# Optimization experiments

Measured on AMD Instinct MI355X. Metric: run time of the kernel, lower is better.

## Reference

```python
import jax, jax.numpy as jnp
import numpy as np

N = 65536       # tokens (voxels)
C = 128         # dim
H = 4           # num_heads
HD = C // H     # head_dim = 32
NUM_WIN = 1024  # number of windows


def setup_inputs() -> dict:
    key = jax.random.key(0)
    k1, k2, k3, k4 = jax.random.split(key, 4)
    x = jax.random.normal(k1, (N, C), dtype=jnp.float32)
    w_qkv = jax.random.normal(k2, (3 * C, C), dtype=jnp.float32) * 0.02
    w_proj = jax.random.normal(k3, (C, C), dtype=jnp.float32) * 0.02
    b_proj = jnp.zeros((C,), dtype=jnp.float32)
    batch_win_inds = jnp.sort(jax.random.randint(k4, (N,), 0, NUM_WIN)).astype(jnp.int32)
    counts = jax.ops.segment_sum(jnp.ones((N,), jnp.int32), batch_win_inds, num_segments=NUM_WIN)
    offsets = jnp.concatenate([jnp.zeros((1,), jnp.int32), jnp.cumsum(counts)]).astype(jnp.int32)
    return {"x": x, "w_qkv": w_qkv, "w_proj": w_proj, "b_proj": b_proj,
            "batch_win_inds": batch_win_inds, "offsets": offsets, "counts": counts}


def reference(x, w_qkv, w_proj, b_proj, batch_win_inds, offsets, counts):
    # qkv projection (no bias), split, per-head reshape
    qkv = (x @ w_qkv.T).reshape(N, 3, H, HD)          # [N,3,H,HD]
    q = jax.nn.relu(qkv[:, 0])                        # [N,H,HD]
    k = jax.nn.relu(qkv[:, 1])                        # [N,H,HD]
    v = qkv[:, 2]                                     # [N,H,HD]

    kv = jax.ops.segment_sum(
        jnp.einsum('nhc,nhd->nhcd', k, v), batch_win_inds, num_segments=NUM_WIN)
    # per-window key sum s[w,h,c]
    s = jax.ops.segment_sum(k, batch_win_inds, num_segments=NUM_WIN)

    y = jnp.einsum('nhc,nhcd->nhd', q, kv[batch_win_inds])
    z = jnp.sum(s[batch_win_inds] * q, axis=-1, keepdims=True)
    y = y / (z + 1e-6)

    y = y.reshape(N, C)
    return y @ w_proj.T + b_proj
```

## Files before the change

kernel.cpp:

```cpp
#include <hip/hip_runtime.h>

namespace {
constexpr int C     = 128;
constexpr int T     = 64;
constexpr int BLK   = 512;
constexpr int NWIN  = 1024;
constexpr int KVSTR = 40;
constexpr int KTSTR = 72;
constexpr int YNSTR = 136;
constexpr int WSPN  = 131072;
constexpr size_t QN = (size_t)65536 * 128;
}

typedef __attribute__((ext_vector_type(8))) short bf16x8;
typedef __attribute__((ext_vector_type(4))) short sh4;
typedef __attribute__((ext_vector_type(4))) float f32x4;

__device__ __forceinline__ short bf16rne(float f) {
    unsigned u = __float_as_uint(f);
    u += 0x7fffu + ((u >> 16) & 1u);
    return (short)(u >> 16);
}
__device__ __forceinline__ float bf16f(short h) {
    return __uint_as_float(((unsigned)(unsigned short)h) << 16);
}
__device__ __forceinline__ void split1(float f, short& hi, short& lo) {
    hi = bf16rne(f);
    lo = bf16rne(f - bf16f(hi));
}

__global__ void prep_weights(const float* __restrict__ wqkv,
                             const float* __restrict__ wproj,
                             short* __restrict__ wsp) {
    const int i = blockIdx.x * 256 + threadIdx.x;
    const float f = (i < 49152) ? wqkv[i] : wproj[i - 49152];
    short hi, lo;
    split1(f, hi, lo);
    wsp[i] = hi;
    wsp[65536 + i] = lo;
}

__global__ __launch_bounds__(BLK, 2)
void qkv_gemm(const float* __restrict__ x,
              const short* __restrict__ wsp,
              short* __restrict__ qws,
              short* __restrict__ kws,
              short* __restrict__ vws)
{
    __shared__ __align__(16) short xh[64 * YNSTR];
    __shared__ __align__(16) short xl[64 * YNSTR];

    const int tid = threadIdx.x;
    const int wv = tid >> 6, ln = tid & 63;
    const int fr = ln & 15, fg = ln >> 4;
    const int r0 = blockIdx.x * 64;

#pragma unroll
    for (int it = 0; it < 2; ++it) {
        const int i = tid + it * BLK;
        const int t = i >> 4, c8 = (i & 15) << 3;
        const float* p = x + (size_t)(r0 + t) * C + c8;
        const float4 a = *(const float4*)p;
        const float4 b = *(const float4*)(p + 4);
        const float f[8] = {a.x, a.y, a.z, a.w, b.x, b.y, b.z, b.w};
        bf16x8 hi, lo;
#pragma unroll
        for (int u = 0; u < 8; ++u) { short h_, l_; split1(f[u], h_, l_); hi[u] = h_; lo[u] = l_; }
        *(bf16x8*)(xh + t * YNSTR + c8) = hi;
        *(bf16x8*)(xl + t * YNSTR + c8) = lo;
    }
    __syncthreads();

    f32x4 acc[3][4];
#pragma unroll
    for (int ni = 0; ni < 3; ++ni)
#pragma unroll
        for (int m = 0; m < 4; ++m) acc[ni][m] = f32x4{0.f, 0.f, 0.f, 0.f};

#pragma unroll
    for (int ksi = 0; ksi < 4; ++ksi) {
        const int koff = ksi * 32 + fg * 8;
        bf16x8 ahi[4], alo[4];
#pragma unroll
        for (int m = 0; m < 4; ++m) {
            const int row = m * 16 + fr;
            ahi[m] = *(const bf16x8*)(xh + row * YNSTR + koff);
            alo[m] = *(const bf16x8*)(xl + row * YNSTR + koff);
        }
#pragma unroll
        for (int ni = 0; ni < 3; ++ni) {
            const int idx = ((3 * wv + ni) * 16 + fr) * C + koff;
            const bf16x8 bhi = *(const bf16x8*)(wsp + idx);
            const bf16x8 blo = *(const bf16x8*)(wsp + 65536 + idx);
#pragma unroll
            for (int m = 0; m < 4; ++m) {
                acc[ni][m] = __builtin_amdgcn_mfma_f32_16x16x32_bf16(ahi[m], bhi, acc[ni][m], 0, 0, 0);
                acc[ni][m] = __builtin_amdgcn_mfma_f32_16x16x32_bf16(ahi[m], blo, acc[ni][m], 0, 0, 0);
                acc[ni][m] = __builtin_amdgcn_mfma_f32_16x16x32_bf16(alo[m], bhi, acc[ni][m], 0, 0, 0);
            }
        }
    }

    const int trow = tid >> 3;
    const int toff = (tid & 7) << 4;
#pragma unroll
    for (int p = 0; p < 3; ++p) {
        __syncthreads();
#pragma unroll
        for (int ni = 0; ni < 3; ++ni) {
            const int ti = 3 * wv + ni;
            if ((ti >> 3) == p) {
                const int lc = (ti - 8 * p) * 16 + fr;
                const bool rl = (p < 2);
#pragma unroll
                for (int m = 0; m < 4; ++m)
#pragma unroll
                    for (int e = 0; e < 4; ++e) {
                        float v = acc[ni][m][e];
                        if (rl) v = fmaxf(v, 0.f);
                        xh[(m * 16 + fg * 4 + e) * YNSTR + lc] = bf16rne(v);
                    }
            }
        }
        __syncthreads();
        short* dst = (p == 0) ? qws : ((p == 1) ? kws : vws);
        const bf16x8 o0 = *(const bf16x8*)(xh + trow * YNSTR + toff);
        const bf16x8 o1 = *(const bf16x8*)(xh + trow * YNSTR + toff + 8);
        *(bf16x8*)(dst + (size_t)(r0 + trow) * C + toff) = o0;
        *(bf16x8*)(dst + (size_t)(r0 + trow) * C + toff + 8) = o1;
    }
}

__global__ __launch_bounds__(BLK, 2)
void sla_win(const short* __restrict__ qws,
             const short* __restrict__ kws,
             const short* __restrict__ vws,
             const short* __restrict__ wsp,
             const float* __restrict__ bproj,
             const int*   __restrict__ offsets,
             float*       __restrict__ out)
{
    __shared__ __align__(16) short kT[C * KTSTR];
    __shared__ __align__(16) short vT[C * KTSTR];
    __shared__ __align__(16) short yn[T * YNSTR];
    __shared__ __align__(16) short kvs[4 * 32 * KVSTR];
    __shared__ float ss[C];

    const int win = blockIdx.x;
    const int beg = offsets[win];
    const int cnt = offsets[win + 1] - beg;
    if (cnt <= 0) return;
    const int nch = (cnt + T - 1) / T;

    const int tid = threadIdx.x;
    const int wv = tid >> 6, ln = tid & 63;
    const int fr = ln & 15, fg = ln >> 4;
    const int aH = wv >> 1, tw = wv & 1;

    f32x4 kvacc[2] = {{0.f,0.f,0.f,0.f},{0.f,0.f,0.f,0.f}};
    f32x4 sacc = {0.f, 0.f, 0.f, 0.f};
    bf16x8 ones;
#pragma unroll
    for (int u = 0; u < 8; ++u) ones[u] = (short)0x3F80;

    for (int c0 = 0; c0 < nch; ++c0) {
        const int t0 = c0 * T;
        const int tc = (cnt - t0 < T) ? (cnt - t0) : T;

#pragma unroll
        for (int it = 0; it < 2; ++it) {
            const int i = tid + it * BLK;
            const int t = i >> 4, c8 = (i & 15) << 3;
            bf16x8 k8, v8;
#pragma unroll
            for (int u = 0; u < 8; ++u) { k8[u] = 0; v8[u] = 0; }
            if (t < tc) {
                k8 = *(const bf16x8*)(kws + (size_t)(beg + t0 + t) * C + c8);
                v8 = *(const bf16x8*)(vws + (size_t)(beg + t0 + t) * C + c8);
            }
#pragma unroll
            for (int u = 0; u < 8; ++u) {
                const int c = c8 + u;
                const int tt = t ^ (((c >> 3) & 7) << 3);
                kT[c * KTSTR + tt] = k8[u];
                vT[c * KTSTR + tt] = v8[u];
            }
        }
        __syncthreads();

        {
#pragma unroll
            for (int kt = 0; kt < 2; ++kt) {
                const int t8 = kt * 32 + fg * 8;
                const int cch = aH * 32 + tw * 16 + fr;
                const bf16x8 a8 = *(const bf16x8*)(kT + cch * KTSTR + (t8 ^ (((cch >> 3) & 7) << 3)));
                sacc = __builtin_amdgcn_mfma_f32_16x16x32_bf16(a8, ones, sacc, 0, 0, 0);
#pragma unroll
                for (int dt = 0; dt < 2; ++dt) {
                    const int dch = aH * 32 + dt * 16 + fr;
                    const bf16x8 b8 = *(const bf16x8*)(vT + dch * KTSTR + (t8 ^ (((dch >> 3) & 7) << 3)));
                    kvacc[dt] = __builtin_amdgcn_mfma_f32_16x16x32_bf16(a8, b8, kvacc[dt], 0, 0, 0);
                }
            }
        }
        if (c0 + 1 < nch) __syncthreads();
    }

    {
#pragma unroll
        for (int dt = 0; dt < 2; ++dt) {
            const int d = dt * 16 + fr;
#pragma unroll
            for (int e = 0; e < 4; ++e) {
                const int c = tw * 16 + fg * 4 + e;
                kvs[aH * (32 * KVSTR) + d * KVSTR + c] = bf16rne(kvacc[dt][e]);
            }
        }
        if (fr == 0) {
#pragma unroll
            for (int e = 0; e < 4; ++e)
                ss[aH * 32 + tw * 16 + fg * 4 + e] = sacc[e];
        }
    }
    __syncthreads();

    for (int c0 = 0; c0 < nch; ++c0) {
        const int t0 = c0 * T;
        const int tc = (cnt - t0 < T) ? (cnt - t0) : T;

        {
            const int a = wv >> 1, mp = wv & 1;
            bf16x8 bfr[2];
#pragma unroll
            for (int dl = 0; dl < 2; ++dl)
                bfr[dl] = *(const bf16x8*)(kvs + a * (32 * KVSTR) + (dl * 16 + fr) * KVSTR + fg * 8);

            const float4 s0 = *(const float4*)(ss + a * 32 + fg * 8);
            const float4 s1 = *(const float4*)(ss + a * 32 + fg * 8 + 4);

            bf16x8 afr[2];
            float zinv[2];
#pragma unroll
            for (int mi = 0; mi < 2; ++mi) {
                const int row = (mp * 2 + mi) * 16 + fr;
                afr[mi] = *(const bf16x8*)(qws + (size_t)(beg + t0 + row) * C + a * 32 + fg * 8);
                float zp = 0.f;
                zp = fmaf(bf16f(afr[mi][0]), s0.x, zp);
                zp = fmaf(bf16f(afr[mi][1]), s0.y, zp);
                zp = fmaf(bf16f(afr[mi][2]), s0.z, zp);
                zp = fmaf(bf16f(afr[mi][3]), s0.w, zp);
                zp = fmaf(bf16f(afr[mi][4]), s1.x, zp);
                zp = fmaf(bf16f(afr[mi][5]), s1.y, zp);
                zp = fmaf(bf16f(afr[mi][6]), s1.z, zp);
                zp = fmaf(bf16f(afr[mi][7]), s1.w, zp);
                zp += __shfl_xor(zp, 16);
                zp += __shfl_xor(zp, 32);
                zinv[mi] = 1.f / (zp + 1e-6f);
            }
            f32x4 acc[2][2];
#pragma unroll
            for (int mi = 0; mi < 2; ++mi)
#pragma unroll
                for (int dl = 0; dl < 2; ++dl) {
                    acc[mi][dl] = f32x4{0.f, 0.f, 0.f, 0.f};
                    acc[mi][dl] = __builtin_amdgcn_mfma_f32_16x16x32_bf16(afr[mi], bfr[dl], acc[mi][dl], 0, 0, 0);
                }
#pragma unroll
            for (int mi = 0; mi < 2; ++mi)
#pragma unroll
                for (int e = 0; e < 4; ++e) {
                    const float zt = __shfl(zinv[mi], fg * 4 + e);
                    const int t = (mp * 2 + mi) * 16 + fg * 4 + e;
#pragma unroll
                    for (int dl = 0; dl < 2; ++dl) {
                        const int ch = a * 32 + dl * 16 + fr;
                        yn[t * YNSTR + ch] = bf16rne(acc[mi][dl][e] * zt);
                    }
                }
        }
        __syncthreads();

        {
            f32x4 acc[4];
#pragma unroll
            for (int m = 0; m < 4; ++m) acc[m] = f32x4{0.f, 0.f, 0.f, 0.f};
#pragma unroll
            for (int ksi = 0; ksi < 4; ++ksi) {
                const int koff = ksi * 32 + fg * 8;
                bf16x8 a8[4];
#pragma unroll
                for (int m = 0; m < 4; ++m) {
                    const int row = m * 16 + fr;
                    a8[m] = *(const bf16x8*)(yn + row * YNSTR + koff);
                }
                const int idx = (384 + wv * 16 + fr) * C + koff;
                const bf16x8 bhi = *(const bf16x8*)(wsp + idx);
                const bf16x8 blo = *(const bf16x8*)(wsp + 65536 + idx);
#pragma unroll
                for (int m = 0; m < 4; ++m) {
                    acc[m] = __builtin_amdgcn_mfma_f32_16x16x32_bf16(a8[m], bhi, acc[m], 0, 0, 0);
                    acc[m] = __builtin_amdgcn_mfma_f32_16x16x32_bf16(a8[m], blo, acc[m], 0, 0, 0);
                }
            }
            const int ch = wv * 16 + fr;
            const float b = bproj[ch];
#pragma unroll
            for (int m = 0; m < 4; ++m)
#pragma unroll
                for (int e = 0; e < 4; ++e) {
                    const int t = m * 16 + fg * 4 + e;
                    if (t < tc)
                        out[(size_t)(beg + t0 + t) * C + ch] = acc[m][e] + b;
                }
        }
        if (c0 + 1 < nch) __syncthreads();
    }
}

__global__ __launch_bounds__(BLK, 2)
void sla6(const float* __restrict__ x, const float* __restrict__ bproj,
          const int* __restrict__ offsets, const short* __restrict__ wsp,
          short* __restrict__ qws, float* __restrict__ out)
{
    __shared__ __align__(16) short xs_hi[T * C];
    __shared__ __align__(16) short xs_lo[T * C];
    __shared__ __align__(16) short kT[C * T];
    __shared__ __align__(16) short vTy[C * T];
    __shared__ __align__(16) short kvs[4 * 32 * KVSTR];
    __shared__ float ss[C];

    const int win = blockIdx.x;
    const int beg = offsets[win];
    const int cnt = offsets[win + 1] - beg;
    if (cnt <= 0) return;
    const int nch = (cnt + T - 1) / T;

    const int tid = threadIdx.x;
    const int wv = tid >> 6, ln = tid & 63;
    const int fr = ln & 15, fg = ln >> 4;

    auto loadB = [&](int row512, int koff, bf16x8& bhi, bf16x8& blo) {
        const int idx = row512 * C + koff;
        bhi = *(const bf16x8*)(wsp + idx);
        blo = *(const bf16x8*)(wsp + 65536 + idx);
    };
    auto stage = [&](int t0, int tc) {
#pragma unroll
        for (int it = 0; it < 2; ++it) {
            const int i = tid + it * BLK;
            const int t = i >> 4, c8 = (i & 15) << 3;
            float4 a = {0.f, 0.f, 0.f, 0.f}, b = {0.f, 0.f, 0.f, 0.f};
            if (t < tc) {
                const float* p = x + (size_t)(beg + t0 + t) * C + c8;
                a = *(const float4*)p;
                b = *(const float4*)(p + 4);
            }
            const float f[8] = {a.x, a.y, a.z, a.w, b.x, b.y, b.z, b.w};
            bf16x8 hi, lo;
#pragma unroll
            for (int u = 0; u < 8; ++u) { short h_, l_; split1(f[u], h_, l_); hi[u] = h_; lo[u] = l_; }
            const int s = t * C + (c8 ^ ((t & 7) << 3));
            *(bf16x8*)(xs_hi + s) = hi;
            *(bf16x8*)(xs_lo + s) = lo;
        }
    };

    const int aH = wv >> 1, tw = wv & 1;
    f32x4 kvacc[2] = {{0.f,0.f,0.f,0.f},{0.f,0.f,0.f,0.f}};
    f32x4 sacc = {0.f, 0.f, 0.f, 0.f};
    bf16x8 ones;
#pragma unroll
    for (int u = 0; u < 8; ++u) ones[u] = (short)0x3F80;

    for (int c0 = 0; c0 < nch; ++c0) {
        const int t0 = c0 * T;
        const int tc = (cnt - t0 < T) ? (cnt - t0) : T;
        stage(t0, tc);
        __syncthreads();
        sh4 qreg[4];
        {
            f32x4 acc[2][4];
#pragma unroll
            for (int ni = 0; ni < 2; ++ni)
#pragma unroll
                for (int m = 0; m < 4; ++m) acc[ni][m] = f32x4{0.f, 0.f, 0.f, 0.f};
#pragma unroll
            for (int ksi = 0; ksi < 4; ++ksi) {
                const int koff = ksi * 32 + fg * 8;
                bf16x8 ahi[4], alo[4];
#pragma unroll
                for (int m = 0; m < 4; ++m) {
                    const int row = m * 16 + fr;
                    const int s = row * C + (koff ^ ((row & 7) << 3));
                    ahi[m] = *(const bf16x8*)(xs_hi + s);
                    alo[m] = *(const bf16x8*)(xs_lo + s);
                }
#pragma unroll
                for (int ni = 0; ni < 2; ++ni) {
                    bf16x8 bhi, blo;
                    loadB(128 + (2 * wv + ni) * 16 + fr, koff, bhi, blo);
#pragma unroll
                    for (int m = 0; m < 4; ++m) {
                        acc[ni][m] = __builtin_amdgcn_mfma_f32_16x16x32_bf16(ahi[m], bhi, acc[ni][m], 0, 0, 0);
                        acc[ni][m] = __builtin_amdgcn_mfma_f32_16x16x32_bf16(ahi[m], blo, acc[ni][m], 0, 0, 0);
                        acc[ni][m] = __builtin_amdgcn_mfma_f32_16x16x32_bf16(alo[m], bhi, acc[ni][m], 0, 0, 0);
                    }
                }
            }
#pragma unroll
            for (int ni = 0; ni < 2; ++ni) {
                const int nt = 2 * wv + ni;
                const bool isk = (nt < 8);
                const int ch = (isk ? nt : nt - 8) * 16 + fr;
                short* dst = isk ? kT : vTy;
#pragma unroll
                for (int m = 0; m < 4; ++m) {
                    sh4 h4;
#pragma unroll
                    for (int e = 0; e < 4; ++e) {
                        float v = acc[ni][m][e];
                        if (isk) v = fmaxf(v, 0.f);
                        h4[e] = bf16rne(v);
                    }
                    const int tb = m * 16 + fg * 4;
                    *(sh4*)(dst + ch * T + (tb ^ ((ch & 7) << 3))) = h4;
                }
            }
        }
        {
            f32x4 acc[4];
#pragma unroll
            for (int m = 0; m < 4; ++m) acc[m] = f32x4{0.f, 0.f, 0.f, 0.f};
#pragma unroll
            for (int ksi = 0; ksi < 4; ++ksi) {
                const int koff = ksi * 32 + fg * 8;
                bf16x8 ahi[4], alo[4];
#pragma unroll
                for (int m = 0; m < 4; ++m) {
                    const int row = m * 16 + fr;
                    const int s = row * C + (koff ^ ((row & 7) << 3));
                    ahi[m] = *(const bf16x8*)(xs_hi + s);
                    alo[m] = *(const bf16x8*)(xs_lo + s);
                }
                bf16x8 bhi, blo;
                loadB(wv * 16 + fr, koff, bhi, blo);
#pragma unroll
                for (int m = 0; m < 4; ++m) {
                    acc[m] = __builtin_amdgcn_mfma_f32_16x16x32_bf16(ahi[m], bhi, acc[m], 0, 0, 0);
                    acc[m] = __builtin_amdgcn_mfma_f32_16x16x32_bf16(ahi[m], blo, acc[m], 0, 0, 0);
                    acc[m] = __builtin_amdgcn_mfma_f32_16x16x32_bf16(alo[m], bhi, acc[m], 0, 0, 0);
                }
            }
#pragma unroll
            for (int m = 0; m < 4; ++m)
#pragma unroll
                for (int e = 0; e < 4; ++e)
                    qreg[m][e] = bf16rne(fmaxf(acc[m][e], 0.f));
        }
        __syncthreads();
        {
            const int ch = wv * 16 + fr;
            if (nch == 1) {
#pragma unroll
                for (int m = 0; m < 4; ++m)
#pragma unroll
                    for (int e = 0; e < 4; ++e) {
                        const int t = m * 16 + fg * 4 + e;
                        xs_hi[t * C + (ch ^ ((t & 7) << 3))] = qreg[m][e];
                    }
            } else {
#pragma unroll
                for (int m = 0; m < 4; ++m)
#pragma unroll
                    for (int e = 0; e < 4; ++e) {
                        const int t = m * 16 + fg * 4 + e;
                        if (t < tc)
                            qws[(size_t)(beg + t0 + t) * C + ch] = qreg[m][e];
                    }
            }
        }
        {
#pragma unroll
            for (int kt = 0; kt < 2; ++kt) {
                const int t8 = kt * 32 + fg * 8;
                const int cch = aH * 32 + tw * 16 + fr;
                const bf16x8 a8 = *(const bf16x8*)(kT + cch * T + (t8 ^ ((cch & 7) << 3)));
                sacc = __builtin_amdgcn_mfma_f32_16x16x32_bf16(a8, ones, sacc, 0, 0, 0);
#pragma unroll
                for (int dt = 0; dt < 2; ++dt) {
                    const int dch = aH * 32 + dt * 16 + fr;
                    const bf16x8 b8 = *(const bf16x8*)(vTy + dch * T + (t8 ^ ((dch & 7) << 3)));
                    kvacc[dt] = __builtin_amdgcn_mfma_f32_16x16x32_bf16(a8, b8, kvacc[dt], 0, 0, 0);
                }
            }
        }
        if (c0 + 1 < nch) __syncthreads();
    }
    {
#pragma unroll
        for (int dt = 0; dt < 2; ++dt) {
            const int d = dt * 16 + fr;
#pragma unroll
            for (int e = 0; e < 4; ++e) {
                const int c = tw * 16 + fg * 4 + e;
                kvs[aH * (32 * KVSTR) + d * KVSTR + c] = bf16rne(kvacc[dt][e]);
            }
        }
        if (fr == 0) {
#pragma unroll
            for (int e = 0; e < 4; ++e)
                ss[aH * 32 + tw * 16 + fg * 4 + e] = sacc[e];
        }
    }
    __syncthreads();
    for (int c0 = 0; c0 < nch; ++c0) {
        const int t0 = c0 * T;
        const int tc = (cnt - t0 < T) ? (cnt - t0) : T;
        {
            const int a = wv >> 1, mp = wv & 1;
            bf16x8 bfr[2];
#pragma unroll
            for (int dl = 0; dl < 2; ++dl)
                bfr[dl] = *(const bf16x8*)(kvs + a * (32 * KVSTR) + (dl * 16 + fr) * KVSTR + fg * 8);
            const float4 s0 = *(const float4*)(ss + a * 32 + fg * 8);
            const float4 s1 = *(const float4*)(ss + a * 32 + fg * 8 + 4);
            bf16x8 afr[2];
            float zinv[2];
#pragma unroll
            for (int mi = 0; mi < 2; ++mi) {
                const int row = (mp * 2 + mi) * 16 + fr;
                if (nch == 1)
                    afr[mi] = *(const bf16x8*)(xs_hi + row * C + ((a * 32 + fg * 8) ^ ((row & 7) << 3)));
                else
                    afr[mi] = *(const bf16x8*)(qws + (size_t)(beg + t0 + row) * C + a * 32 + fg * 8);
                float zp = 0.f;
                zp = fmaf(bf16f(afr[mi][0]), s0.x, zp);
                zp = fmaf(bf16f(afr[mi][1]), s0.y, zp);
                zp = fmaf(bf16f(afr[mi][2]), s0.z, zp);
                zp = fmaf(bf16f(afr[mi][3]), s0.w, zp);
                zp = fmaf(bf16f(afr[mi][4]), s1.x, zp);
                zp = fmaf(bf16f(afr[mi][5]), s1.y, zp);
                zp = fmaf(bf16f(afr[mi][6]), s1.z, zp);
                zp = fmaf(bf16f(afr[mi][7]), s1.w, zp);
                zp += __shfl_xor(zp, 16);
                zp += __shfl_xor(zp, 32);
                zinv[mi] = 1.f / (zp + 1e-6f);
            }
            f32x4 acc[2][2];
#pragma unroll
            for (int mi = 0; mi < 2; ++mi)
#pragma unroll
                for (int dl = 0; dl < 2; ++dl) {
                    acc[mi][dl] = f32x4{0.f, 0.f, 0.f, 0.f};
                    acc[mi][dl] = __builtin_amdgcn_mfma_f32_16x16x32_bf16(afr[mi], bfr[dl], acc[mi][dl], 0, 0, 0);
                }
#pragma unroll
            for (int mi = 0; mi < 2; ++mi)
#pragma unroll
                for (int e = 0; e < 4; ++e) {
                    const float zt = __shfl(zinv[mi], fg * 4 + e);
                    const int t = (mp * 2 + mi) * 16 + fg * 4 + e;
#pragma unroll
                    for (int dl = 0; dl < 2; ++dl) {
                        const int ch = a * 32 + dl * 16 + fr;
                        vTy[t * C + (ch ^ ((t & 7) << 3))] = bf16rne(acc[mi][dl][e] * zt);
                    }
                }
        }
        __syncthreads();
        {
            f32x4 acc[4];
#pragma unroll
            for (int m = 0; m < 4; ++m) acc[m] = f32x4{0.f, 0.f, 0.f, 0.f};
#pragma unroll
            for (int ksi = 0; ksi < 4; ++ksi) {
                const int koff = ksi * 32 + fg * 8;
                bf16x8 a8[4];
#pragma unroll
                for (int m = 0; m < 4; ++m) {
                    const int row = m * 16 + fr;
                    a8[m] = *(const bf16x8*)(vTy + row * C + (koff ^ ((row & 7) << 3)));
                }
                bf16x8 bhi, blo;
                loadB(384 + wv * 16 + fr, koff, bhi, blo);
#pragma unroll
                for (int m = 0; m < 4; ++m) {
                    acc[m] = __builtin_amdgcn_mfma_f32_16x16x32_bf16(a8[m], bhi, acc[m], 0, 0, 0);
                    acc[m] = __builtin_amdgcn_mfma_f32_16x16x32_bf16(a8[m], blo, acc[m], 0, 0, 0);
                }
            }
            const int ch = wv * 16 + fr;
            const float b = bproj[ch];
#pragma unroll
            for (int m = 0; m < 4; ++m)
#pragma unroll
                for (int e = 0; e < 4; ++e) {
                    const int t = m * 16 + fg * 4 + e;
                    if (t < tc)
                        out[(size_t)(beg + t0 + t) * C + ch] = acc[m][e] + b;
                }
        }
        if (c0 + 1 < nch) __syncthreads();
    }
}

extern "C" void kernel_launch(void* const* d_in, const int* in_sizes, int n_in,
                              void* d_out, int out_size, void* d_ws, size_t ws_size,
                              hipStream_t stream)
{
    const float* x       = (const float*)d_in[0];
    const float* wqkv    = (const float*)d_in[1];
    const float* wproj   = (const float*)d_in[2];
    const float* bproj   = (const float*)d_in[3];
    const int*   offsets = (const int*)d_in[5];
    float* out = (float*)d_out;
    short* wsp = (short*)d_ws;

    const size_t need_split = ((size_t)WSPN + 3 * QN) * sizeof(short);
    const size_t need_sla6  = ((size_t)WSPN + QN) * sizeof(short);

    if (ws_size >= need_split) {
        short* qws = wsp + WSPN;
        short* kws = qws + QN;
        short* vws = kws + QN;
        hipLaunchKernelGGL(prep_weights, dim3(256), dim3(256), 0, stream, wqkv, wproj, wsp);
        hipLaunchKernelGGL(qkv_gemm, dim3(65536 / 64), dim3(BLK), 0, stream,
                           x, wsp, qws, kws, vws);
        hipLaunchKernelGGL(sla_win, dim3(NWIN), dim3(BLK), 0, stream,
                           qws, kws, vws, wsp, bproj, offsets, out);
    } else if (ws_size >= need_sla6) {
        hipLaunchKernelGGL(prep_weights, dim3(256), dim3(256), 0, stream, wqkv, wproj, wsp);
        hipLaunchKernelGGL(sla6, dim3(NWIN), dim3(BLK), 0, stream,
                           x, bproj, offsets, wsp, wsp + WSPN, out);
    }
}
```

Before: 77.98 us.

## Keep QKV weight fragments in registers and process four row chunks per block

The QKV GEMM kernel now loads each wave's bf16 hi/lo weight fragments into registers once and reuses them across four 64-row chunks, so each block covers 256 rows and the grid shrinks to a quarter. The epilogue writes Q and K together using both shared buffers, then V, which cuts the number of barrier-separated phases. This removes repeated global weight loads per 64 rows. In exchange it uses many more registers (96 bf16x8 vectors), which could lower occupancy or cause spills, and it launches fewer blocks.

```diff
diff --git a/kernel.cpp b/kernel.cpp
--- a/kernel.cpp
+++ b/kernel.cpp
@@ -53,81 +53,115 @@
     const int tid = threadIdx.x;
     const int wv = tid >> 6, ln = tid & 63;
     const int fr = ln & 15, fg = ln >> 4;
-    const int r0 = blockIdx.x * 64;
-
-#pragma unroll
-    for (int it = 0; it < 2; ++it) {
-        const int i = tid + it * BLK;
-        const int t = i >> 4, c8 = (i & 15) << 3;
-        const float* p = x + (size_t)(r0 + t) * C + c8;
-        const float4 a = *(const float4*)p;
-        const float4 b = *(const float4*)(p + 4);
-        const float f[8] = {a.x, a.y, a.z, a.w, b.x, b.y, b.z, b.w};
-        bf16x8 hi, lo;
-#pragma unroll
-        for (int u = 0; u < 8; ++u) { short h_, l_; split1(f[u], h_, l_); hi[u] = h_; lo[u] = l_; }
-        *(bf16x8*)(xh + t * YNSTR + c8) = hi;
-        *(bf16x8*)(xl + t * YNSTR + c8) = lo;
-    }
-    __syncthreads();
-
-    f32x4 acc[3][4];
+    const int r0 = blockIdx.x * 256;
+
+    bf16x8 Bh[3][4], Bl[3][4];
 #pragma unroll
     for (int ni = 0; ni < 3; ++ni)
 #pragma unroll
-        for (int m = 0; m < 4; ++m) acc[ni][m] = f32x4{0.f, 0.f, 0.f, 0.f};
-
-#pragma unroll
-    for (int ksi = 0; ksi < 4; ++ksi) {
-        const int koff = ksi * 32 + fg * 8;
-        bf16x8 ahi[4], alo[4];
-#pragma unroll
-        for (int m = 0; m < 4; ++m) {
-            const int row = m * 16 + fr;
-            ahi[m] = *(const bf16x8*)(xh + row * YNSTR + koff);
-            alo[m] = *(const bf16x8*)(xl + row * YNSTR + koff);
-        }
-#pragma unroll
-        for (int ni = 0; ni < 3; ++ni) {
-            const int idx = ((3 * wv + ni) * 16 + fr) * C + koff;
-            const bf16x8 bhi = *(const bf16x8*)(wsp + idx);
-            const bf16x8 blo = *(const bf16x8*)(wsp + 65536 + idx);
-#pragma unroll
-            for (int m = 0; m < 4; ++m) {
-                acc[ni][m] = __builtin_amdgcn_mfma_f32_16x16x32_bf16(ahi[m], bhi, acc[ni][m], 0, 0, 0);
-                acc[ni][m] = __builtin_amdgcn_mfma_f32_16x16x32_bf16(ahi[m], blo, acc[ni][m], 0, 0, 0);
-                acc[ni][m] = __builtin_amdgcn_mfma_f32_16x16x32_bf16(alo[m], bhi, acc[ni][m], 0, 0, 0);
-            }
-        }
-    }
+        for (int ksi = 0; ksi < 4; ++ksi) {
+            const int idx = ((3 * wv + ni) * 16 + fr) * C + ksi * 32 + fg * 8;
+            Bh[ni][ksi] = *(const bf16x8*)(wsp + idx);
+            Bl[ni][ksi] = *(const bf16x8*)(wsp + 65536 + idx);
+        }
 
     const int trow = tid >> 3;
     const int toff = (tid & 7) << 4;
-#pragma unroll
-    for (int p = 0; p < 3; ++p) {
-        __syncthreads();
+
+    for (int ch = 0; ch < 4; ++ch) {
+        const int rbase = r0 + ch * 64;
+        if (ch) __syncthreads();
+
+#pragma unroll
+        for (int it = 0; it < 2; ++it) {
+            const int i = tid + it * BLK;
+            const int t = i >> 4, c8 = (i & 15) << 3;
+            const float* p = x + (size_t)(rbase + t) * C + c8;
+            const float4 a = *(const float4*)p;
+            const float4 b = *(const float4*)(p + 4);
+            const float f[8] = {a.x, a.y, a.z, a.w, b.x, b.y, b.z, b.w};
+            bf16x8 hi, lo;
+#pragma unroll
+            for (int u = 0; u < 8; ++u) { short h_, l_; split1(f[u], h_, l_); hi[u] = h_; lo[u] = l_; }
+            *(bf16x8*)(xh + t * YNSTR + c8) = hi;
+            *(bf16x8*)(xl + t * YNSTR + c8) = lo;
+        }
+        __syncthreads();
+
+        f32x4 acc[3][4];
+#pragma unroll
+        for (int ni = 0; ni < 3; ++ni)
+#pragma unroll
+            for (int m = 0; m < 4; ++m) acc[ni][m] = f32x4{0.f, 0.f, 0.f, 0.f};
+
+#pragma unroll
+        for (int ksi = 0; ksi < 4; ++ksi) {
+            const int koff = ksi * 32 + fg * 8;
+            bf16x8 ahi[4], alo[4];
+#pragma unroll
+            for (int m = 0; m < 4; ++m) {
+                const int row = m * 16 + fr;
+                ahi[m] = *(const bf16x8*)(xh + row * YNSTR + koff);
+                alo[m] = *(const bf16x8*)(xl + row * YNSTR + koff);
+            }
+#pragma unroll
+            for (int ni = 0; ni < 3; ++ni)
+#pragma unroll
+                for (int m = 0; m < 4; ++m) {
+                    acc[ni][m] = __builtin_amdgcn_mfma_f32_16x16x32_bf16(ahi[m], Bh[ni][ksi], acc[ni][m], 0, 0, 0);
+                    acc[ni][m] = __builtin_amdgcn_mfma_f32_16x16x32_bf16(ahi[m], Bl[ni][ksi], acc[ni][m], 0, 0, 0);
+                    acc[ni][m] = __builtin_amdgcn_mfma_f32_16x16x32_bf16(alo[m], Bh[ni][ksi], acc[ni][m], 0, 0, 0);
+                }
+        }
+        __syncthreads();
+
 #pragma unroll
         for (int ni = 0; ni < 3; ++ni) {
             const int ti = 3 * wv + ni;
-            if ((ti >> 3) == p) {
-                const int lc = (ti - 8 * p) * 16 + fr;
-                const bool rl = (p < 2);
+            const int p = ti >> 3;
+            if (p < 2) {
+                short* buf = (p == 0) ? xh : xl;
+                const int lc = (ti & 7) * 16 + fr;
 #pragma unroll
                 for (int m = 0; m < 4; ++m)
 #pragma unroll
-                    for (int e = 0; e < 4; ++e) {
-                        float v = acc[ni][m][e];
-                        if (rl) v = fmaxf(v, 0.f);
-                        xh[(m * 16 + fg * 4 + e) * YNSTR + lc] = bf16rne(v);
-                    }
-            }
-        }
-        __syncthreads();
-        short* dst = (p == 0) ? qws : ((p == 1) ? kws : vws);
-        const bf16x8 o0 = *(const bf16x8*)(xh + trow * YNSTR + toff);
-        const bf16x8 o1 = *(const bf16x8*)(xh + trow * YNSTR + toff + 8);
-        *(bf16x8*)(dst + (size_t)(r0 + trow) * C + toff) = o0;
-        *(bf16x8*)(dst + (size_t)(r0 + trow) * C + toff + 8) = o1;
+                    for (int e = 0; e < 4; ++e)
+                        buf[(m * 16 + fg * 4 + e) * YNSTR + lc] =
+                            bf16rne(fmaxf(acc[ni][m][e], 0.f));
+            }
+        }
+        __syncthreads();
+        {
+            const bf16x8 q0 = *(const bf16x8*)(xh + trow * YNSTR + toff);
+            const bf16x8 q1 = *(const bf16x8*)(xh + trow * YNSTR + toff + 8);
+            const bf16x8 k0 = *(const bf16x8*)(xl + trow * YNSTR + toff);
+            const bf16x8 k1 = *(const bf16x8*)(xl + trow * YNSTR + toff + 8);
+            *(bf16x8*)(qws + (size_t)(rbase + trow) * C + toff)     = q0;
+            *(bf16x8*)(qws + (size_t)(rbase + trow) * C + toff + 8) = q1;
+            *(bf16x8*)(kws + (size_t)(rbase + trow) * C + toff)     = k0;
+            *(bf16x8*)(kws + (size_t)(rbase + trow) * C + toff + 8) = k1;
+        }
+        __syncthreads();
+
+#pragma unroll
+        for (int ni = 0; ni < 3; ++ni) {
+            const int ti = 3 * wv + ni;
+            if ((ti >> 3) == 2) {
+                const int lc = (ti & 7) * 16 + fr;
+#pragma unroll
+                for (int m = 0; m < 4; ++m)
+#pragma unroll
+                    for (int e = 0; e < 4; ++e)
+                        xh[(m * 16 + fg * 4 + e) * YNSTR + lc] = bf16rne(acc[ni][m][e]);
+            }
+        }
+        __syncthreads();
+        {
+            const bf16x8 v0 = *(const bf16x8*)(xh + trow * YNSTR + toff);
+            const bf16x8 v1 = *(const bf16x8*)(xh + trow * YNSTR + toff + 8);
+            *(bf16x8*)(vws + (size_t)(rbase + trow) * C + toff)     = v0;
+            *(bf16x8*)(vws + (size_t)(rbase + trow) * C + toff + 8) = v1;
+        }
     }
 }
 
@@ -624,7 +658,7 @@
         short* kws = qws + QN;
         short* vws = kws + QN;
         hipLaunchKernelGGL(prep_weights, dim3(256), dim3(256), 0, stream, wqkv, wproj, wsp);
-        hipLaunchKernelGGL(qkv_gemm, dim3(65536 / 64), dim3(BLK), 0, stream,
+        hipLaunchKernelGGL(qkv_gemm, dim3(65536 / 256), dim3(BLK), 0, stream,
                            x, wsp, qws, kws, vws);
         hipLaunchKernelGGL(sla_win, dim3(NWIN), dim3(BLK), 0, stream,
                            qws, kws, vws, wsp, bproj, offsets, out);
```

New measurement: 71.64 us, median of 2. -8.1%, faster.

## Store K/V transposed per 64-token chunk from QKV GEMM for window kernel

Applied to the files above, without the earlier changes.

The QKV GEMM now writes K and V directly in a channel-major layout per 64-token global chunk, so the window kernel can load them with vector reads and vector LDS stores instead of scalar transposes. Each GEMM block now processes 128 rows in two 64-row passes and stages Q through a separate shared buffer. The window kernel iterates over the global chunks overlapping each window and masks out tokens outside it, which can mean extra chunk loads when windows straddle chunk boundaries. Halving the GEMM grid and adding shared memory may reduce occupancy.

```diff
diff --git a/kernel.cpp b/kernel.cpp
--- a/kernel.cpp
+++ b/kernel.cpp
@@ -6,7 +6,6 @@
 constexpr int BLK   = 512;
 constexpr int NWIN  = 1024;
 constexpr int KVSTR = 40;
-constexpr int KTSTR = 72;
 constexpr int YNSTR = 136;
 constexpr int WSPN  = 131072;
 constexpr size_t QN = (size_t)65536 * 128;
@@ -41,107 +40,134 @@
 }
 
 __global__ __launch_bounds__(BLK, 2)
-void qkv_gemm(const float* __restrict__ x,
-              const short* __restrict__ wsp,
-              short* __restrict__ qws,
-              short* __restrict__ kws,
-              short* __restrict__ vws)
+void qkv_t(const float* __restrict__ x,
+           const short* __restrict__ wsp,
+           short* __restrict__ qws,
+           short* __restrict__ ktg,
+           short* __restrict__ vtg)
 {
     __shared__ __align__(16) short xh[64 * YNSTR];
     __shared__ __align__(16) short xl[64 * YNSTR];
+    __shared__ __align__(16) short qs[64 * YNSTR];
 
     const int tid = threadIdx.x;
     const int wv = tid >> 6, ln = tid & 63;
     const int fr = ln & 15, fg = ln >> 4;
-    const int r0 = blockIdx.x * 64;
-
-#pragma unroll
-    for (int it = 0; it < 2; ++it) {
-        const int i = tid + it * BLK;
-        const int t = i >> 4, c8 = (i & 15) << 3;
-        const float* p = x + (size_t)(r0 + t) * C + c8;
-        const float4 a = *(const float4*)p;
-        const float4 b = *(const float4*)(p + 4);
-        const float f[8] = {a.x, a.y, a.z, a.w, b.x, b.y, b.z, b.w};
-        bf16x8 hi, lo;
-#pragma unroll
-        for (int u = 0; u < 8; ++u) { short h_, l_; split1(f[u], h_, l_); hi[u] = h_; lo[u] = l_; }
-        *(bf16x8*)(xh + t * YNSTR + c8) = hi;
-        *(bf16x8*)(xl + t * YNSTR + c8) = lo;
-    }
-    __syncthreads();
-
-    f32x4 acc[3][4];
-#pragma unroll
-    for (int ni = 0; ni < 3; ++ni)
-#pragma unroll
-        for (int m = 0; m < 4; ++m) acc[ni][m] = f32x4{0.f, 0.f, 0.f, 0.f};
-
-#pragma unroll
-    for (int ksi = 0; ksi < 4; ++ksi) {
-        const int koff = ksi * 32 + fg * 8;
-        bf16x8 ahi[4], alo[4];
-#pragma unroll
-        for (int m = 0; m < 4; ++m) {
-            const int row = m * 16 + fr;
-            ahi[m] = *(const bf16x8*)(xh + row * YNSTR + koff);
-            alo[m] = *(const bf16x8*)(xl + row * YNSTR + koff);
-        }
-#pragma unroll
-        for (int ni = 0; ni < 3; ++ni) {
-            const int idx = ((3 * wv + ni) * 16 + fr) * C + koff;
-            const bf16x8 bhi = *(const bf16x8*)(wsp + idx);
-            const bf16x8 blo = *(const bf16x8*)(wsp + 65536 + idx);
-#pragma unroll
-            for (int m = 0; m < 4; ++m) {
-                acc[ni][m] = __builtin_amdgcn_mfma_f32_16x16x32_bf16(ahi[m], bhi, acc[ni][m], 0, 0, 0);
-                acc[ni][m] = __builtin_amdgcn_mfma_f32_16x16x32_bf16(ahi[m], blo, acc[ni][m], 0, 0, 0);
-                acc[ni][m] = __builtin_amdgcn_mfma_f32_16x16x32_bf16(alo[m], bhi, acc[ni][m], 0, 0, 0);
-            }
-        }
-    }
-
+    const int r0 = blockIdx.x * 128;
+
+    const int st_t = tid >> 4;
+    const int st_c8 = (tid & 15) << 3;
     const int trow = tid >> 3;
     const int toff = (tid & 7) << 4;
-#pragma unroll
-    for (int p = 0; p < 3; ++p) {
+
+    auto stage = [&](int rbase) {
+#pragma unroll
+        for (int it = 0; it < 2; ++it) {
+            const int t = st_t + it * 32;
+            const float* p = x + (size_t)(rbase + t) * C + st_c8;
+            const float4 a = *(const float4*)p;
+            const float4 b = *(const float4*)(p + 4);
+            const float f[8] = {a.x, a.y, a.z, a.w, b.x, b.y, b.z, b.w};
+            bf16x8 hi, lo;
+#pragma unroll
+            for (int u = 0; u < 8; ++u) { short h_, l_; split1(f[u], h_, l_); hi[u] = h_; lo[u] = l_; }
+            *(bf16x8*)(xh + t * YNSTR + st_c8) = hi;
+            *(bf16x8*)(xl + t * YNSTR + st_c8) = lo;
+        }
+    };
+
+    stage(r0);
+    __syncthreads();
+
+    for (int c = 0; c < 2; ++c) {
+        const int rbase = r0 + c * 64;
+        const int chunk = rbase >> 6;
+
+        f32x4 acc[3][4];
+#pragma unroll
+        for (int ni = 0; ni < 3; ++ni)
+#pragma unroll
+            for (int m = 0; m < 4; ++m) acc[ni][m] = f32x4{0.f, 0.f, 0.f, 0.f};
+
+#pragma unroll
+        for (int ksi = 0; ksi < 4; ++ksi) {
+            const int koff = ksi * 32 + fg * 8;
+            bf16x8 ahi[4], alo[4];
+#pragma unroll
+            for (int m = 0; m < 4; ++m) {
+                const int row = m * 16 + fr;
+                ahi[m] = *(const bf16x8*)(xh + row * YNSTR + koff);
+                alo[m] = *(const bf16x8*)(xl + row * YNSTR + koff);
+            }
+#pragma unroll
+            for (int ni = 0; ni < 3; ++ni) {
+                const int idx = ((3 * wv + ni) * 16 + fr) * C + koff;
+                const bf16x8 bhi = *(const bf16x8*)(wsp + idx);
+                const bf16x8 blo = *(const bf16x8*)(wsp + 65536 + idx);
+#pragma unroll
+                for (int m = 0; m < 4; ++m) {
+                    acc[ni][m] = __builtin_amdgcn_mfma_f32_16x16x32_bf16(ahi[m], bhi, acc[ni][m], 0, 0, 0);
+                    acc[ni][m] = __builtin_amdgcn_mfma_f32_16x16x32_bf16(ahi[m], blo, acc[ni][m], 0, 0, 0);
+                    acc[ni][m] = __builtin_amdgcn_mfma_f32_16x16x32_bf16(alo[m], bhi, acc[ni][m], 0, 0, 0);
+                }
+            }
+        }
         __syncthreads();
+
 #pragma unroll
         for (int ni = 0; ni < 3; ++ni) {
             const int ti = 3 * wv + ni;
-            if ((ti >> 3) == p) {
-                const int lc = (ti - 8 * p) * 16 + fr;
-                const bool rl = (p < 2);
+            if (ti < 8) {
+                const int lc = ti * 16 + fr;
 #pragma unroll
                 for (int m = 0; m < 4; ++m)
+#pragma unroll
+                    for (int e = 0; e < 4; ++e)
+                        qs[(m * 16 + fg * 4 + e) * YNSTR + lc] =
+                            bf16rne(fmaxf(acc[ni][m][e], 0.f));
+            } else {
+                const bool isk = (ti < 16);
+                short* dst = isk ? ktg : vtg;
+                const int ch = (ti & 7) * 16 + fr;
+#pragma unroll
+                for (int m = 0; m < 4; ++m) {
+                    sh4 h4;
 #pragma unroll
                     for (int e = 0; e < 4; ++e) {
                         float v = acc[ni][m][e];
-                        if (rl) v = fmaxf(v, 0.f);
-                        xh[(m * 16 + fg * 4 + e) * YNSTR + lc] = bf16rne(v);
+                        if (isk) v = fmaxf(v, 0.f);
+                        h4[e] = bf16rne(v);
                     }
+                    *(sh4*)(dst + (size_t)chunk * 8192 + ch * 64 + m * 16 + fg * 4) = h4;
+                }
             }
         }
         __syncthreads();
-        short* dst = (p == 0) ? qws : ((p == 1) ? kws : vws);
-        const bf16x8 o0 = *(const bf16x8*)(xh + trow * YNSTR + toff);
-        const bf16x8 o1 = *(const bf16x8*)(xh + trow * YNSTR + toff + 8);
-        *(bf16x8*)(dst + (size_t)(r0 + trow) * C + toff) = o0;
-        *(bf16x8*)(dst + (size_t)(r0 + trow) * C + toff + 8) = o1;
+
+        {
+            const bf16x8 q0 = *(const bf16x8*)(qs + trow * YNSTR + toff);
+            const bf16x8 q1 = *(const bf16x8*)(qs + trow * YNSTR + toff + 8);
+            *(bf16x8*)(qws + (size_t)(rbase + trow) * C + toff)     = q0;
+            *(bf16x8*)(qws + (size_t)(rbase + trow) * C + toff + 8) = q1;
+        }
+        if (c == 0) {
+            stage(r0 + 64);
+            __syncthreads();
+        }
     }
 }
 
 __global__ __launch_bounds__(BLK, 2)
-void sla_win(const short* __restrict__ qws,
-             const short* __restrict__ kws,
-             const short* __restrict__ vws,
-             const short* __restrict__ wsp,
-             const float* __restrict__ bproj,
-             const int*   __restrict__ offsets,
-             float*       __restrict__ out)
+void sla_y(const short* __restrict__ qws,
+           const short* __restrict__ ktg,
+           const short* __restrict__ vtg,
+           const short* __restrict__ wsp,
+           const float* __restrict__ bproj,
+           const int*   __restrict__ offsets,
+           float*       __restrict__ out)
 {
-    __shared__ __align__(16) short kT[C * KTSTR];
-    __shared__ __align__(16) short vT[C * KTSTR];
+    __shared__ __align__(16) short kT[C * 64];
+    __shared__ __align__(16) short vT[C * 64];
     __shared__ __align__(16) short yn[T * YNSTR];
     __shared__ __align__(16) short kvs[4 * 32 * KVSTR];
     __shared__ float ss[C];
@@ -150,7 +176,10 @@
     const int beg = offsets[win];
     const int cnt = offsets[win + 1] - beg;
     if (cnt <= 0) return;
+    const int end = beg + cnt;
     const int nch = (cnt + T - 1) / T;
+    const int ck0 = beg >> 6;
+    const int ck1 = (end - 1) >> 6;
 
     const int tid = threadIdx.x;
     const int wv = tid >> 6, ln = tid & 63;
@@ -163,28 +192,21 @@
 #pragma unroll
     for (int u = 0; u < 8; ++u) ones[u] = (short)0x3F80;
 
-    for (int c0 = 0; c0 < nch; ++c0) {
-        const int t0 = c0 * T;
-        const int tc = (cnt - t0 < T) ? (cnt - t0) : T;
-
+    for (int ck = ck0; ck <= ck1; ++ck) {
 #pragma unroll
         for (int it = 0; it < 2; ++it) {
             const int i = tid + it * BLK;
-            const int t = i >> 4, c8 = (i & 15) << 3;
-            bf16x8 k8, v8;
-#pragma unroll
-            for (int u = 0; u < 8; ++u) { k8[u] = 0; v8[u] = 0; }
-            if (t < tc) {
-                k8 = *(const bf16x8*)(kws + (size_t)(beg + t0 + t) * C + c8);
-                v8 = *(const bf16x8*)(vws + (size_t)(beg + t0 + t) * C + c8);
-            }
+            const int ch = i >> 3, o8 = (i & 7) << 3;
+            bf16x8 k8 = *(const bf16x8*)(ktg + (size_t)ck * 8192 + ch * 64 + o8);
+            bf16x8 v8 = *(const bf16x8*)(vtg + (size_t)ck * 8192 + ch * 64 + o8);
+            const int tokbase = ck * 64 + o8;
 #pragma unroll
             for (int u = 0; u < 8; ++u) {
-                const int c = c8 + u;
-                const int tt = t ^ (((c >> 3) & 7) << 3);
-                kT[c * KTSTR + tt] = k8[u];
-                vT[c * KTSTR + tt] = v8[u];
-            }
+                if ((unsigned)(tokbase + u - beg) >= (unsigned)cnt) { k8[u] = 0; v8[u] = 0; }
+            }
+            const int od = o8 ^ ((ch & 7) << 3);
+            *(bf16x8*)(kT + ch * 64 + od) = k8;
+            *(bf16x8*)(vT + ch * 64 + od) = v8;
         }
         __syncthreads();
 
@@ -193,17 +215,17 @@
             for (int kt = 0; kt < 2; ++kt) {
                 const int t8 = kt * 32 + fg * 8;
                 const int cch = aH * 32 + tw * 16 + fr;
-                const bf16x8 a8 = *(const bf16x8*)(kT + cch * KTSTR + (t8 ^ (((cch >> 3) & 7) << 3)));
+                const bf16x8 a8 = *(const bf16x8*)(kT + cch * 64 + (t8 ^ ((cch & 7) << 3)));
                 sacc = __builtin_amdgcn_mfma_f32_16x16x32_bf16(a8, ones, sacc, 0, 0, 0);
 #pragma unroll
                 for (int dt = 0; dt < 2; ++dt) {
                     const int dch = aH * 32 + dt * 16 + fr;
-                    const bf16x8 b8 = *(const bf16x8*)(vT + dch * KTSTR + (t8 ^ (((dch >> 3) & 7) << 3)));
+                    const bf16x8 b8 = *(const bf16x8*)(vT + dch * 64 + (t8 ^ ((dch & 7) << 3)));
                     kvacc[dt] = __builtin_amdgcn_mfma_f32_16x16x32_bf16(a8, b8, kvacc[dt], 0, 0, 0);
                 }
             }
         }
-        if (c0 + 1 < nch) __syncthreads();
+        if (ck < ck1) __syncthreads();
     }
 
     {
@@ -621,13 +643,13 @@
 
     if (ws_size >= need_split) {
         short* qws = wsp + WSPN;
-        short* kws = qws + QN;
-        short* vws = kws + QN;
+        short* ktg = qws + QN;
+        short* vtg = ktg + QN;
         hipLaunchKernelGGL(prep_weights, dim3(256), dim3(256), 0, stream, wqkv, wproj, wsp);
-        hipLaunchKernelGGL(qkv_gemm, dim3(65536 / 64), dim3(BLK), 0, stream,
-                           x, wsp, qws, kws, vws);
-        hipLaunchKernelGGL(sla_win, dim3(NWIN), dim3(BLK), 0, stream,
-                           qws, kws, vws, wsp, bproj, offsets, out);
+        hipLaunchKernelGGL(qkv_t, dim3(65536 / 128), dim3(BLK), 0, stream,
+                           x, wsp, qws, ktg, vtg);
+        hipLaunchKernelGGL(sla_y, dim3(NWIN), dim3(BLK), 0, stream,
+                           qws, ktg, vtg, wsp, bproj, offsets, out);
     } else if (ws_size >= need_sla6) {
         hipLaunchKernelGGL(prep_weights, dim3(256), dim3(256), 0, stream, wqkv, wproj, wsp);
         hipLaunchKernelGGL(sla6, dim3(NWIN), dim3(BLK), 0, stream,
```

Result: slower. 80.28 us (+3.0%).
